# Kernel optimization log

Measured on AMD Instinct MI355X. Metric: run time of the kernel, lower is better.

## Reference

```python
import jax, jax.numpy as jnp
import numpy as np

B, T, H, QS = 32, 4096, 512, 512

def setup_inputs() -> dict:
    key = jax.random.key(0)
    k1, k2, k3, k4, k5 = jax.random.split(key, 5)
    query = jax.random.normal(k1, (B, 1, QS), dtype=jnp.float32)
    precomputed_key = jax.random.normal(k2, (B, T, H), dtype=jnp.float32)
    value = jax.random.normal(k3, (B, T, H), dtype=jnp.float32)
    mask = jnp.ones((B, T), dtype=bool)  # unused in original forward
    Wq = jax.random.normal(k4, (H, QS), dtype=jnp.float32) * (1.0 / np.sqrt(QS))
    We = jax.random.normal(k5, (H,), dtype=jnp.float32) * (1.0 / np.sqrt(H))
    return {"query": query, "precomputed_key": precomputed_key, "value": value,
            "mask": mask, "Wq": Wq, "We": We}

def reference(query, precomputed_key, value, mask, Wq, We):
    # query_layer: Linear(query_size -> hidden, no bias): x @ Wq.T
    q = jnp.einsum('bqs,hs->bqh', query, Wq)              # [B,1,H]
    # energy: tanh(q + key) then Linear(hidden -> 1, no bias), squeeze
    scores = jnp.einsum('bth,h->bt', jnp.tanh(q + precomputed_key), We)  # [B,T]
    alphas = jax.nn.softmax(scores, axis=1)               # [B,T]
    # bmm(alphas[B,1,T], value[B,T,D]) -> [B,1,D]
    context = jnp.einsum('bt,btd->bd', alphas, value)[:, None, :]
    return context, alphas
```

## Files before the change

### kernel.cpp

```cpp
#include <hip/hip_runtime.h>
#include <math.h>

#define BB 32
#define TT 4096
#define HH 512
#define QQS 512
#define TS 64
#define CH 64

#define TANH_K 2.8853900817779268f
#define LOG2E  1.4426950408889634f

__device__ inline float fast_exp2(float x) {
#if __has_builtin(__builtin_amdgcn_exp2f)
    return __builtin_amdgcn_exp2f(x);
#else
    return exp2f(x);
#endif
}
__device__ inline float fast_rcp(float x) {
#if __has_builtin(__builtin_amdgcn_rcpf)
    return __builtin_amdgcn_rcpf(x);
#else
    return 1.f / x;
#endif
}

__device__ inline float wave_reduce_sum(float v) {
#pragma unroll
    for (int off = 32; off > 0; off >>= 1) v += __shfl_xor(v, off, 64);
    return v;
}

__global__ void qproj_kernel(const float* __restrict__ query,
                             const float* __restrict__ Wq,
                             float* __restrict__ qout) {
    int wid  = (blockIdx.x * blockDim.x + threadIdx.x) >> 6;
    int lane = threadIdx.x & 63;
    int b = wid >> 9;
    int h = wid & (HH - 1);
    const float4* qr = (const float4*)(query + (size_t)b * QQS);
    const float4* wr = (const float4*)(Wq + (size_t)h * QQS);
    float4 a0 = qr[lane],      w0 = wr[lane];
    float4 a1 = qr[lane + 64], w1 = wr[lane + 64];
    float acc = a0.x * w0.x + a0.y * w0.y + a0.z * w0.z + a0.w * w0.w
              + a1.x * w1.x + a1.y * w1.y + a1.z * w1.z + a1.w * w1.w;
    acc = wave_reduce_sum(acc);
    if (lane == 0) qout[wid] = acc;
}

__device__ inline float tanh_term(float k, float qc, float w, float p) {
    float e = fast_exp2(fmaf(k, TANH_K, qc));
    float r = fast_rcp(e + 1.f);
    float th = fmaf(-2.f, r, 1.f);
    return fmaf(th, w, p);
}

__global__ __launch_bounds__(256) void fused_kernel(
        const float* __restrict__ key, const float* __restrict__ value,
        const float* __restrict__ qb,  const float* __restrict__ We,
        float* __restrict__ alphas, float* __restrict__ zbuf,
        float* __restrict__ part) {
    __shared__ float e_lds[CH];
    __shared__ float4 ctx_lds[4][HH / 4];

    int b = blockIdx.x / TS, c = blockIdx.x % TS;
    int tid = threadIdx.x, w = tid >> 6, lane = tid & 63;
    size_t row0 = (size_t)b * TT + (size_t)c * CH;

    const float4* qv = (const float4*)(qb + (size_t)b * HH);
    const float4* wv = (const float4*)We;
    float4 q0 = qv[lane], q1 = qv[lane + 64];
    float4 w0 = wv[lane], w1 = wv[lane + 64];
    q0.x *= TANH_K; q0.y *= TANH_K; q0.z *= TANH_K; q0.w *= TANH_K;
    q1.x *= TANH_K; q1.y *= TANH_K; q1.z *= TANH_K; q1.w *= TANH_K;

    const float4* kb4 = (const float4*)(key + row0 * HH);
    const float4* vb4 = (const float4*)(value + row0 * HH);

    float4 accA = make_float4(0.f, 0.f, 0.f, 0.f);
    float4 accB = make_float4(0.f, 0.f, 0.f, 0.f);

    for (int j = 0; j < 16; j += 2) {
        int r0 = w + 4 * j, r1 = r0 + 4;
        const float4* kp0 = kb4 + (size_t)r0 * (HH / 4);
        const float4* kp1 = kb4 + (size_t)r1 * (HH / 4);
        const float4* vp0 = vb4 + (size_t)r0 * (HH / 4);
        const float4* vp1 = vb4 + (size_t)r1 * (HH / 4);
        float4 ka0 = kp0[lane], kc0 = kp0[lane + 64];
        float4 ka1 = kp1[lane], kc1 = kp1[lane + 64];
        float4 va0 = vp0[lane], vc0 = vp0[lane + 64];
        float4 va1 = vp1[lane], vc1 = vp1[lane + 64];

        float p0 = 0.f, p1 = 0.f;
        p0 = tanh_term(ka0.x, q0.x, w0.x, p0);
        p0 = tanh_term(ka0.y, q0.y, w0.y, p0);
        p0 = tanh_term(ka0.z, q0.z, w0.z, p0);
        p0 = tanh_term(ka0.w, q0.w, w0.w, p0);
        p0 = tanh_term(kc0.x, q1.x, w1.x, p0);
        p0 = tanh_term(kc0.y, q1.y, w1.y, p0);
        p0 = tanh_term(kc0.z, q1.z, w1.z, p0);
        p0 = tanh_term(kc0.w, q1.w, w1.w, p0);
        p1 = tanh_term(ka1.x, q0.x, w0.x, p1);
        p1 = tanh_term(ka1.y, q0.y, w0.y, p1);
        p1 = tanh_term(ka1.z, q0.z, w0.z, p1);
        p1 = tanh_term(ka1.w, q0.w, w0.w, p1);
        p1 = tanh_term(kc1.x, q1.x, w1.x, p1);
        p1 = tanh_term(kc1.y, q1.y, w1.y, p1);
        p1 = tanh_term(kc1.z, q1.z, w1.z, p1);
        p1 = tanh_term(kc1.w, q1.w, w1.w, p1);

        float a0 = __shfl_xor(p0, 32, 64);
        float a1 = __shfl_xor(p1, 32, 64);
        float ws = (lane < 32) ? (p0 + a0) : (p1 + a1);
#pragma unroll
        for (int off = 16; off > 0; off >>= 1) ws += __shfl_xor(ws, off, 64);
        float s0 = __shfl(ws, 0, 64);
        float s1 = __shfl(ws, 32, 64);

        float e0 = fast_exp2(s0 * LOG2E);
        float e1 = fast_exp2(s1 * LOG2E);
        if (lane == 0) { e_lds[r0] = e0; e_lds[r1] = e1; }

        accA.x = fmaf(e0, va0.x, accA.x); accA.y = fmaf(e0, va0.y, accA.y);
        accA.z = fmaf(e0, va0.z, accA.z); accA.w = fmaf(e0, va0.w, accA.w);
        accB.x = fmaf(e0, vc0.x, accB.x); accB.y = fmaf(e0, vc0.y, accB.y);
        accB.z = fmaf(e0, vc0.z, accB.z); accB.w = fmaf(e0, vc0.w, accB.w);
        accA.x = fmaf(e1, va1.x, accA.x); accA.y = fmaf(e1, va1.y, accA.y);
        accA.z = fmaf(e1, va1.z, accA.z); accA.w = fmaf(e1, va1.w, accA.w);
        accB.x = fmaf(e1, vc1.x, accB.x); accB.y = fmaf(e1, vc1.y, accB.y);
        accB.z = fmaf(e1, vc1.z, accB.z); accB.w = fmaf(e1, vc1.w, accB.w);
    }

    ctx_lds[w][lane] = accA;
    ctx_lds[w][lane + 64] = accB;
    __syncthreads();

    if (tid < 128) {
        float4 t0 = ctx_lds[0][tid], t1 = ctx_lds[1][tid];
        float4 t2 = ctx_lds[2][tid], t3 = ctx_lds[3][tid];
        float4 t;
        t.x = (t0.x + t1.x) + (t2.x + t3.x);
        t.y = (t0.y + t1.y) + (t2.y + t3.y);
        t.z = (t0.z + t1.z) + (t2.z + t3.z);
        t.w = (t0.w + t1.w) + (t2.w + t3.w);
        ((float4*)(part + ((size_t)c * BB + b) * HH))[tid] = t;
    } else if (tid < 192) {
        int l = tid - 128;
        float e = e_lds[l];
        float z = wave_reduce_sum(e);
        if (l == 0) zbuf[b * TS + c] = z;
        if (l < CH / 4)
            ((float4*)(alphas + row0))[l] = ((const float4*)e_lds)[l];
    }
}

__global__ void finalize_kernel(const float* __restrict__ zbuf,
                                const float* __restrict__ part,
                                float* __restrict__ alphas,
                                float* __restrict__ ctx) {
    int tid = threadIdx.x, lane = tid & 63;
    int b = (blockIdx.x < BB) ? blockIdx.x : ((blockIdx.x - BB) >> 1);

    float z = zbuf[b * TS + lane];
    float Z = wave_reduce_sum(z);
    float invZ = fast_rcp(Z);

    if (blockIdx.x < BB) {
        float4* ap = (float4*)(alphas + (size_t)b * TT);
#pragma unroll
        for (int i = 0; i < 4; ++i) {
            int idx = tid + i * 256;
            float4 a = ap[idx];
            a.x *= invZ; a.y *= invZ; a.z *= invZ; a.w *= invZ;
            ap[idx] = a;
        }
    } else {
        int d = ((blockIdx.x - BB) & 1) * 256 + tid;
        float s = 0.f;
#pragma unroll 8
        for (int c2 = 0; c2 < TS; ++c2)
            s += part[((size_t)c2 * BB + b) * HH + d];
        ctx[(size_t)b * HH + d] = s * invZ;
    }
}

extern "C" void kernel_launch(void* const* d_in, const int* in_sizes, int n_in,
                              void* d_out, int out_size, void* d_ws, size_t ws_size,
                              hipStream_t stream) {
    const float* query = (const float*)d_in[0];
    const float* key   = (const float*)d_in[1];
    const float* value = (const float*)d_in[2];
    const float* Wq    = (const float*)d_in[4];
    const float* We    = (const float*)d_in[5];

    float* ctx    = (float*)d_out;
    float* alphas = (float*)d_out + BB * HH;

    float* qbuf   = (float*)d_ws;
    float* zbuf   = qbuf + BB * HH;
    float* part   = zbuf + BB * TS;

    qproj_kernel<<<(BB * HH) / 4, 256, 0, stream>>>(query, Wq, qbuf);
    fused_kernel<<<BB * TS, 256, 0, stream>>>(key, value, qbuf, We, alphas, zbuf, part);
    finalize_kernel<<<BB + 2 * BB, 256, 0, stream>>>(zbuf, part, alphas, ctx);
}
```

Before: 114.7 us.

## Give each wave its own 32-row chunk with register double-buffered loads

Each wave now handles a contiguous 32-row chunk on its own, instead of four waves sharing a 64-row chunk. This removes the LDS reduction and the __syncthreads barrier at the end of the block. Key and value rows are loaded one pair ahead into two register buffers, so memory latency overlaps with the tanh and exp math. The cost is that the number of context partials doubles, so finalize must sum twice as many partials, and the extra buffers raise register pressure.

```diff
diff --git a/kernel.cpp b/kernel.cpp
--- a/kernel.cpp
+++ b/kernel.cpp
@@ -5,8 +5,8 @@
 #define TT 4096
 #define HH 512
 #define QQS 512
-#define TS 64
-#define CH 64
+#define WCH 32
+#define NCH (TT / WCH)
 
 #define TANH_K 2.8853900817779268f
 #define LOG2E  1.4426950408889634f
@@ -49,11 +49,75 @@
     if (lane == 0) qout[wid] = acc;
 }
 
-__device__ inline float tanh_term(float k, float qc, float w, float p) {
+__device__ __forceinline__ float tanh_term(float k, float qc, float w, float p) {
     float e = fast_exp2(fmaf(k, TANH_K, qc));
     float r = fast_rcp(e + 1.f);
     float th = fmaf(-2.f, r, 1.f);
     return fmaf(th, w, p);
+}
+
+struct Buf {
+    float4 k0a, k0b, k1a, k1b;
+    float4 v0a, v0b, v1a, v1b;
+};
+
+__device__ __forceinline__ void load_pair(const float4* kb4, const float4* vb4,
+                                          int p, int lane, Buf& B) {
+    const float4* kp0 = kb4 + (size_t)(2 * p)     * (HH / 4);
+    const float4* kp1 = kb4 + (size_t)(2 * p + 1) * (HH / 4);
+    const float4* vp0 = vb4 + (size_t)(2 * p)     * (HH / 4);
+    const float4* vp1 = vb4 + (size_t)(2 * p + 1) * (HH / 4);
+    B.k0a = kp0[lane]; B.k0b = kp0[lane + 64];
+    B.k1a = kp1[lane]; B.k1b = kp1[lane + 64];
+    B.v0a = vp0[lane]; B.v0b = vp0[lane + 64];
+    B.v1a = vp1[lane]; B.v1b = vp1[lane + 64];
+}
+
+__device__ __forceinline__ void comp_pair(const Buf& B, int p, int lane,
+                                          const float4& q0, const float4& q1,
+                                          const float4& w0, const float4& w1,
+                                          float4& accA, float4& accB,
+                                          float& z, float& ev) {
+    float p0 = 0.f, p1 = 0.f;
+    p0 = tanh_term(B.k0a.x, q0.x, w0.x, p0);
+    p0 = tanh_term(B.k0a.y, q0.y, w0.y, p0);
+    p0 = tanh_term(B.k0a.z, q0.z, w0.z, p0);
+    p0 = tanh_term(B.k0a.w, q0.w, w0.w, p0);
+    p0 = tanh_term(B.k0b.x, q1.x, w1.x, p0);
+    p0 = tanh_term(B.k0b.y, q1.y, w1.y, p0);
+    p0 = tanh_term(B.k0b.z, q1.z, w1.z, p0);
+    p0 = tanh_term(B.k0b.w, q1.w, w1.w, p0);
+    p1 = tanh_term(B.k1a.x, q0.x, w0.x, p1);
+    p1 = tanh_term(B.k1a.y, q0.y, w0.y, p1);
+    p1 = tanh_term(B.k1a.z, q0.z, w0.z, p1);
+    p1 = tanh_term(B.k1a.w, q0.w, w0.w, p1);
+    p1 = tanh_term(B.k1b.x, q1.x, w1.x, p1);
+    p1 = tanh_term(B.k1b.y, q1.y, w1.y, p1);
+    p1 = tanh_term(B.k1b.z, q1.z, w1.z, p1);
+    p1 = tanh_term(B.k1b.w, q1.w, w1.w, p1);
+
+    float a0 = __shfl_xor(p0, 32, 64);
+    float a1 = __shfl_xor(p1, 32, 64);
+    float ws = (lane < 32) ? (p0 + a0) : (p1 + a1);
+#pragma unroll
+    for (int off = 16; off > 0; off >>= 1) ws += __shfl_xor(ws, off, 64);
+    float s0 = __shfl(ws, 0, 64);
+    float s1 = __shfl(ws, 32, 64);
+
+    float e0 = fast_exp2(s0 * LOG2E);
+    float e1 = fast_exp2(s1 * LOG2E);
+    z += e0 + e1;
+    ev = (lane == 2 * p)     ? e0 : ev;
+    ev = (lane == 2 * p + 1) ? e1 : ev;
+
+    accA.x = fmaf(e0, B.v0a.x, accA.x); accA.y = fmaf(e0, B.v0a.y, accA.y);
+    accA.z = fmaf(e0, B.v0a.z, accA.z); accA.w = fmaf(e0, B.v0a.w, accA.w);
+    accB.x = fmaf(e0, B.v0b.x, accB.x); accB.y = fmaf(e0, B.v0b.y, accB.y);
+    accB.z = fmaf(e0, B.v0b.z, accB.z); accB.w = fmaf(e0, B.v0b.w, accB.w);
+    accA.x = fmaf(e1, B.v1a.x, accA.x); accA.y = fmaf(e1, B.v1a.y, accA.y);
+    accA.z = fmaf(e1, B.v1a.z, accA.z); accA.w = fmaf(e1, B.v1a.w, accA.w);
+    accB.x = fmaf(e1, B.v1b.x, accB.x); accB.y = fmaf(e1, B.v1b.y, accB.y);
+    accB.z = fmaf(e1, B.v1b.z, accB.z); accB.w = fmaf(e1, B.v1b.w, accB.w);
 }
 
 __global__ __launch_bounds__(256) void fused_kernel(
@@ -61,12 +125,10 @@
         const float* __restrict__ qb,  const float* __restrict__ We,
         float* __restrict__ alphas, float* __restrict__ zbuf,
         float* __restrict__ part) {
-    __shared__ float e_lds[CH];
-    __shared__ float4 ctx_lds[4][HH / 4];
-
-    int b = blockIdx.x / TS, c = blockIdx.x % TS;
     int tid = threadIdx.x, w = tid >> 6, lane = tid & 63;
-    size_t row0 = (size_t)b * TT + (size_t)c * CH;
+    int b = blockIdx.x >> 5;
+    int c = ((blockIdx.x & 31) << 2) | w;
+    size_t row0 = (size_t)b * TT + (size_t)c * WCH;
 
     const float4* qv = (const float4*)(qb + (size_t)b * HH);
     const float4* wv = (const float4*)We;
@@ -80,79 +142,26 @@
 
     float4 accA = make_float4(0.f, 0.f, 0.f, 0.f);
     float4 accB = make_float4(0.f, 0.f, 0.f, 0.f);
-
-    for (int j = 0; j < 16; j += 2) {
-        int r0 = w + 4 * j, r1 = r0 + 4;
-        const float4* kp0 = kb4 + (size_t)r0 * (HH / 4);
-        const float4* kp1 = kb4 + (size_t)r1 * (HH / 4);
-        const float4* vp0 = vb4 + (size_t)r0 * (HH / 4);
-        const float4* vp1 = vb4 + (size_t)r1 * (HH / 4);
-        float4 ka0 = kp0[lane], kc0 = kp0[lane + 64];
-        float4 ka1 = kp1[lane], kc1 = kp1[lane + 64];
-        float4 va0 = vp0[lane], vc0 = vp0[lane + 64];
-        float4 va1 = vp1[lane], vc1 = vp1[lane + 64];
-
-        float p0 = 0.f, p1 = 0.f;
-        p0 = tanh_term(ka0.x, q0.x, w0.x, p0);
-        p0 = tanh_term(ka0.y, q0.y, w0.y, p0);
-        p0 = tanh_term(ka0.z, q0.z, w0.z, p0);
-        p0 = tanh_term(ka0.w, q0.w, w0.w, p0);
-        p0 = tanh_term(kc0.x, q1.x, w1.x, p0);
-        p0 = tanh_term(kc0.y, q1.y, w1.y, p0);
-        p0 = tanh_term(kc0.z, q1.z, w1.z, p0);
-        p0 = tanh_term(kc0.w, q1.w, w1.w, p0);
-        p1 = tanh_term(ka1.x, q0.x, w0.x, p1);
-        p1 = tanh_term(ka1.y, q0.y, w0.y, p1);
-        p1 = tanh_term(ka1.z, q0.z, w0.z, p1);
-        p1 = tanh_term(ka1.w, q0.w, w0.w, p1);
-        p1 = tanh_term(kc1.x, q1.x, w1.x, p1);
-        p1 = tanh_term(kc1.y, q1.y, w1.y, p1);
-        p1 = tanh_term(kc1.z, q1.z, w1.z, p1);
-        p1 = tanh_term(kc1.w, q1.w, w1.w, p1);
-
-        float a0 = __shfl_xor(p0, 32, 64);
-        float a1 = __shfl_xor(p1, 32, 64);
-        float ws = (lane < 32) ? (p0 + a0) : (p1 + a1);
-#pragma unroll
-        for (int off = 16; off > 0; off >>= 1) ws += __shfl_xor(ws, off, 64);
-        float s0 = __shfl(ws, 0, 64);
-        float s1 = __shfl(ws, 32, 64);
-
-        float e0 = fast_exp2(s0 * LOG2E);
-        float e1 = fast_exp2(s1 * LOG2E);
-        if (lane == 0) { e_lds[r0] = e0; e_lds[r1] = e1; }
-
-        accA.x = fmaf(e0, va0.x, accA.x); accA.y = fmaf(e0, va0.y, accA.y);
-        accA.z = fmaf(e0, va0.z, accA.z); accA.w = fmaf(e0, va0.w, accA.w);
-        accB.x = fmaf(e0, vc0.x, accB.x); accB.y = fmaf(e0, vc0.y, accB.y);
-        accB.z = fmaf(e0, vc0.z, accB.z); accB.w = fmaf(e0, vc0.w, accB.w);
-        accA.x = fmaf(e1, va1.x, accA.x); accA.y = fmaf(e1, va1.y, accA.y);
-        accA.z = fmaf(e1, va1.z, accA.z); accA.w = fmaf(e1, va1.w, accA.w);
-        accB.x = fmaf(e1, vc1.x, accB.x); accB.y = fmaf(e1, vc1.y, accB.y);
-        accB.z = fmaf(e1, vc1.z, accB.z); accB.w = fmaf(e1, vc1.w, accB.w);
+    float z = 0.f, ev = 0.f;
+
+    Buf X, Y;
+    load_pair(kb4, vb4, 0, lane, X);
+    load_pair(kb4, vb4, 1, lane, Y);
+#pragma unroll
+    for (int p = 0; p < 14; p += 2) {
+        comp_pair(X, p, lane, q0, q1, w0, w1, accA, accB, z, ev);
+        load_pair(kb4, vb4, p + 2, lane, X);
+        comp_pair(Y, p + 1, lane, q0, q1, w0, w1, accA, accB, z, ev);
+        load_pair(kb4, vb4, p + 3, lane, Y);
     }
-
-    ctx_lds[w][lane] = accA;
-    ctx_lds[w][lane + 64] = accB;
-    __syncthreads();
-
-    if (tid < 128) {
-        float4 t0 = ctx_lds[0][tid], t1 = ctx_lds[1][tid];
-        float4 t2 = ctx_lds[2][tid], t3 = ctx_lds[3][tid];
-        float4 t;
-        t.x = (t0.x + t1.x) + (t2.x + t3.x);
-        t.y = (t0.y + t1.y) + (t2.y + t3.y);
-        t.z = (t0.z + t1.z) + (t2.z + t3.z);
-        t.w = (t0.w + t1.w) + (t2.w + t3.w);
-        ((float4*)(part + ((size_t)c * BB + b) * HH))[tid] = t;
-    } else if (tid < 192) {
-        int l = tid - 128;
-        float e = e_lds[l];
-        float z = wave_reduce_sum(e);
-        if (l == 0) zbuf[b * TS + c] = z;
-        if (l < CH / 4)
-            ((float4*)(alphas + row0))[l] = ((const float4*)e_lds)[l];
-    }
+    comp_pair(X, 14, lane, q0, q1, w0, w1, accA, accB, z, ev);
+    comp_pair(Y, 15, lane, q0, q1, w0, w1, accA, accB, z, ev);
+
+    if (lane < WCH) alphas[row0 + lane] = ev;
+    if (lane == 0) zbuf[b * NCH + c] = z;
+    float4* pp = (float4*)(part + ((size_t)c * BB + b) * HH);
+    pp[lane] = accA;
+    pp[lane + 64] = accB;
 }
 
 __global__ void finalize_kernel(const float* __restrict__ zbuf,
@@ -162,7 +171,7 @@
     int tid = threadIdx.x, lane = tid & 63;
     int b = (blockIdx.x < BB) ? blockIdx.x : ((blockIdx.x - BB) >> 1);
 
-    float z = zbuf[b * TS + lane];
+    float z = zbuf[b * NCH + lane] + zbuf[b * NCH + 64 + lane];
     float Z = wave_reduce_sum(z);
     float invZ = fast_rcp(Z);
 
@@ -179,7 +188,7 @@
         int d = ((blockIdx.x - BB) & 1) * 256 + tid;
         float s = 0.f;
 #pragma unroll 8
-        for (int c2 = 0; c2 < TS; ++c2)
+        for (int c2 = 0; c2 < NCH; ++c2)
             s += part[((size_t)c2 * BB + b) * HH + d];
         ctx[(size_t)b * HH + d] = s * invZ;
     }
@@ -199,9 +208,9 @@
 
     float* qbuf   = (float*)d_ws;
     float* zbuf   = qbuf + BB * HH;
-    float* part   = zbuf + BB * TS;
+    float* part   = zbuf + BB * NCH;
 
     qproj_kernel<<<(BB * HH) / 4, 256, 0, stream>>>(query, Wq, qbuf);
-    fused_kernel<<<BB * TS, 256, 0, stream>>>(key, value, qbuf, We, alphas, zbuf, part);
+    fused_kernel<<<BB * 32, 256, 0, stream>>>(key, value, qbuf, We, alphas, zbuf, part);
     finalize_kernel<<<BB + 2 * BB, 256, 0, stream>>>(zbuf, part, alphas, ctx);
 }
```

Measured after the change: 130.7 us. 1.14x slower.

## Split fused kernel into score phase then value accumulation over LDS weights

Applied to the files above, without the earlier changes.

Restructures the fused kernel into two phases. First, each wave computes the tanh scores for its key rows and writes the exp weights to LDS. Then, after a barrier, all 256 threads each own two hidden columns and accumulate value rows weighted by those LDS weights. This removes the cross-wave LDS reduction of the context partials and the ctx_lds buffer, cutting register pressure and shared-memory use. The cost is that value loads can no longer overlap with score computation, and there is an extra barrier in the middle.

```diff
diff --git a/kernel.cpp b/kernel.cpp
--- a/kernel.cpp
+++ b/kernel.cpp
@@ -49,7 +49,7 @@
     if (lane == 0) qout[wid] = acc;
 }
 
-__device__ inline float tanh_term(float k, float qc, float w, float p) {
+__device__ __forceinline__ float tanh_term(float k, float qc, float w, float p) {
     float e = fast_exp2(fmaf(k, TANH_K, qc));
     float r = fast_rcp(e + 1.f);
     float th = fmaf(-2.f, r, 1.f);
@@ -62,7 +62,6 @@
         float* __restrict__ alphas, float* __restrict__ zbuf,
         float* __restrict__ part) {
     __shared__ float e_lds[CH];
-    __shared__ float4 ctx_lds[4][HH / 4];
 
     int b = blockIdx.x / TS, c = blockIdx.x % TS;
     int tid = threadIdx.x, w = tid >> 6, lane = tid & 63;
@@ -76,83 +75,58 @@
     q1.x *= TANH_K; q1.y *= TANH_K; q1.z *= TANH_K; q1.w *= TANH_K;
 
     const float4* kb4 = (const float4*)(key + row0 * HH);
-    const float4* vb4 = (const float4*)(value + row0 * HH);
 
-    float4 accA = make_float4(0.f, 0.f, 0.f, 0.f);
-    float4 accB = make_float4(0.f, 0.f, 0.f, 0.f);
-
-    for (int j = 0; j < 16; j += 2) {
-        int r0 = w + 4 * j, r1 = r0 + 4;
+#pragma unroll 2
+    for (int rr = 0; rr < CH / 8; ++rr) {
+        int r0 = rr * 8 + w, r1 = r0 + 4;
         const float4* kp0 = kb4 + (size_t)r0 * (HH / 4);
         const float4* kp1 = kb4 + (size_t)r1 * (HH / 4);
-        const float4* vp0 = vb4 + (size_t)r0 * (HH / 4);
-        const float4* vp1 = vb4 + (size_t)r1 * (HH / 4);
-        float4 ka0 = kp0[lane], kc0 = kp0[lane + 64];
-        float4 ka1 = kp1[lane], kc1 = kp1[lane + 64];
-        float4 va0 = vp0[lane], vc0 = vp0[lane + 64];
-        float4 va1 = vp1[lane], vc1 = vp1[lane + 64];
-
+        float4 ka = kp0[lane], kb_ = kp0[lane + 64];
+        float4 kc = kp1[lane], kd = kp1[lane + 64];
         float p0 = 0.f, p1 = 0.f;
-        p0 = tanh_term(ka0.x, q0.x, w0.x, p0);
-        p0 = tanh_term(ka0.y, q0.y, w0.y, p0);
-        p0 = tanh_term(ka0.z, q0.z, w0.z, p0);
-        p0 = tanh_term(ka0.w, q0.w, w0.w, p0);
-        p0 = tanh_term(kc0.x, q1.x, w1.x, p0);
-        p0 = tanh_term(kc0.y, q1.y, w1.y, p0);
-        p0 = tanh_term(kc0.z, q1.z, w1.z, p0);
-        p0 = tanh_term(kc0.w, q1.w, w1.w, p0);
-        p1 = tanh_term(ka1.x, q0.x, w0.x, p1);
-        p1 = tanh_term(ka1.y, q0.y, w0.y, p1);
-        p1 = tanh_term(ka1.z, q0.z, w0.z, p1);
-        p1 = tanh_term(ka1.w, q0.w, w0.w, p1);
-        p1 = tanh_term(kc1.x, q1.x, w1.x, p1);
-        p1 = tanh_term(kc1.y, q1.y, w1.y, p1);
-        p1 = tanh_term(kc1.z, q1.z, w1.z, p1);
-        p1 = tanh_term(kc1.w, q1.w, w1.w, p1);
-
+        p0 = tanh_term(ka.x, q0.x, w0.x, p0);
+        p0 = tanh_term(ka.y, q0.y, w0.y, p0);
+        p0 = tanh_term(ka.z, q0.z, w0.z, p0);
+        p0 = tanh_term(ka.w, q0.w, w0.w, p0);
+        p0 = tanh_term(kb_.x, q1.x, w1.x, p0);
+        p0 = tanh_term(kb_.y, q1.y, w1.y, p0);
+        p0 = tanh_term(kb_.z, q1.z, w1.z, p0);
+        p0 = tanh_term(kb_.w, q1.w, w1.w, p0);
+        p1 = tanh_term(kc.x, q0.x, w0.x, p1);
+        p1 = tanh_term(kc.y, q0.y, w0.y, p1);
+        p1 = tanh_term(kc.z, q0.z, w0.z, p1);
+        p1 = tanh_term(kc.w, q0.w, w0.w, p1);
+        p1 = tanh_term(kd.x, q1.x, w1.x, p1);
+        p1 = tanh_term(kd.y, q1.y, w1.y, p1);
+        p1 = tanh_term(kd.z, q1.z, w1.z, p1);
+        p1 = tanh_term(kd.w, q1.w, w1.w, p1);
         float a0 = __shfl_xor(p0, 32, 64);
         float a1 = __shfl_xor(p1, 32, 64);
         float ws = (lane < 32) ? (p0 + a0) : (p1 + a1);
 #pragma unroll
         for (int off = 16; off > 0; off >>= 1) ws += __shfl_xor(ws, off, 64);
-        float s0 = __shfl(ws, 0, 64);
-        float s1 = __shfl(ws, 32, 64);
+        if ((lane & 31) == 0)
+            e_lds[(lane < 32) ? r0 : r1] = fast_exp2(ws * LOG2E);
+    }
+    __syncthreads();
 
-        float e0 = fast_exp2(s0 * LOG2E);
-        float e1 = fast_exp2(s1 * LOG2E);
-        if (lane == 0) { e_lds[r0] = e0; e_lds[r1] = e1; }
-
-        accA.x = fmaf(e0, va0.x, accA.x); accA.y = fmaf(e0, va0.y, accA.y);
-        accA.z = fmaf(e0, va0.z, accA.z); accA.w = fmaf(e0, va0.w, accA.w);
-        accB.x = fmaf(e0, vc0.x, accB.x); accB.y = fmaf(e0, vc0.y, accB.y);
-        accB.z = fmaf(e0, vc0.z, accB.z); accB.w = fmaf(e0, vc0.w, accB.w);
-        accA.x = fmaf(e1, va1.x, accA.x); accA.y = fmaf(e1, va1.y, accA.y);
-        accA.z = fmaf(e1, va1.z, accA.z); accA.w = fmaf(e1, va1.w, accA.w);
-        accB.x = fmaf(e1, vc1.x, accB.x); accB.y = fmaf(e1, vc1.y, accB.y);
-        accB.z = fmaf(e1, vc1.z, accB.z); accB.w = fmaf(e1, vc1.w, accB.w);
+    if (w == 0) {
+        float e = e_lds[lane];
+        alphas[row0 + lane] = e;
+        float zz = wave_reduce_sum(e);
+        if (lane == 0) zbuf[b * TS + c] = zz;
     }
 
-    ctx_lds[w][lane] = accA;
-    ctx_lds[w][lane + 64] = accB;
-    __syncthreads();
-
-    if (tid < 128) {
-        float4 t0 = ctx_lds[0][tid], t1 = ctx_lds[1][tid];
-        float4 t2 = ctx_lds[2][tid], t3 = ctx_lds[3][tid];
-        float4 t;
-        t.x = (t0.x + t1.x) + (t2.x + t3.x);
-        t.y = (t0.y + t1.y) + (t2.y + t3.y);
-        t.z = (t0.z + t1.z) + (t2.z + t3.z);
-        t.w = (t0.w + t1.w) + (t2.w + t3.w);
-        ((float4*)(part + ((size_t)c * BB + b) * HH))[tid] = t;
-    } else if (tid < 192) {
-        int l = tid - 128;
-        float e = e_lds[l];
-        float z = wave_reduce_sum(e);
-        if (l == 0) zbuf[b * TS + c] = z;
-        if (l < CH / 4)
-            ((float4*)(alphas + row0))[l] = ((const float4*)e_lds)[l];
+    const float2* vb2 = (const float2*)(value + row0 * HH);
+    float2 acc = make_float2(0.f, 0.f);
+#pragma unroll 8
+    for (int r = 0; r < CH; ++r) {
+        float e = e_lds[r];
+        float2 v = vb2[(size_t)r * (HH / 2) + tid];
+        acc.x = fmaf(e, v.x, acc.x);
+        acc.y = fmaf(e, v.y, acc.y);
     }
+    ((float2*)(part + ((size_t)c * BB + b) * HH))[tid] = acc;
 }
 
 __global__ void finalize_kernel(const float* __restrict__ zbuf,
```

Result: faster. 110.7 us (-3.5%).
